# Kernel optimization log

Measured on AMD Instinct MI355X. Metric: run time of the kernel, lower is better.

Reference implementation:

```python
import jax, jax.numpy as jnp
import numpy as np

N_COG = 72  # 360 / delta_cog
N_RB = 72   # 360 / delta_rb
B, N, H = 64, 512, 128


def setup_inputs() -> dict:
    key = jax.random.key(0)
    k1, k2, k3, k4, k5, k6 = jax.random.split(key, 6)
    h_t = jax.random.normal(k1, (N, B, H), dtype=jnp.float32)
    r_mat = jax.random.randint(k2, (B, N, N), 0, N_RB, dtype=jnp.int32)
    d_mat = jax.random.uniform(k3, (B, N, N), dtype=jnp.float32)
    mask = jax.random.randint(k4, (B, N), 0, 2).astype(jnp.float32)
    cog_mat = jax.random.randint(k5, (B, N, N), 0, N_COG, dtype=jnp.int32)
    domain = jax.random.normal(k6, (N_COG, N_RB), dtype=jnp.float32)
    return {"h_t": h_t, "r_mat": r_mat, "d_mat": d_mat, "mask": mask,
            "cog_mat": cog_mat, "domain": domain}


def reference(h_t, r_mat, d_mat, mask, cog_mat, domain):
    # gather from learnable domain table, subtract distance, relu
    w = jax.nn.relu(domain[cog_mat, r_mat] - d_mat)          # [B, N, N]
    # pairwise mask (applied twice in the original, around normalization)
    m = mask[:, :, None] * mask[:, None, :]                   # [B, N, N]
    w = m * w
    # global-max normalize; torch uses .data.max() (no grad through max)
    w = w / jax.lax.stop_gradient(jnp.max(w))
    w = m * w
    # out[b,i,h] = sum_j w[b,i,j] * h_t[j,b,h]
    return jnp.einsum('bij,jbh->bih', w, h_t)                 # [B, N, H]
```

## Files before the change

kernel.cpp:

```cpp
#include <hip/hip_runtime.h>


#define B_   64
#define N_   512
#define H_   128
#define NCOG 72
#define NRB  72

typedef __bf16 bf16x8 __attribute__((ext_vector_type(8)));
typedef float  f32x4  __attribute__((ext_vector_type(4)));

__device__ __forceinline__ void async_copy16_nt(const void* g, void* l) {
    __builtin_amdgcn_global_load_lds(
        (const __attribute__((address_space(1))) void*)g,
        (__attribute__((address_space(3))) void*)l, 16, 0, 2);
}

__global__ __launch_bounds__(256) void k_transpose(const float* __restrict__ ht,
                                                   __bf16* __restrict__ T) {
    __shared__ __bf16 tile[32][136];
    const int jt = blockIdx.x * 32;
    const int b  = blockIdx.y;
    const int t  = threadIdx.x;
    {
        const int jj = t >> 3;
        const int h0 = (t & 7) << 4;
        const float* src = ht + ((size_t)(jt + jj) * B_ + b) * H_ + h0;
        float4 v0 = *(const float4*)(src + 0);
        float4 v1 = *(const float4*)(src + 4);
        float4 v2 = *(const float4*)(src + 8);
        float4 v3 = *(const float4*)(src + 12);
        __bf16* dst = &tile[jj][h0];
        dst[0]=(__bf16)v0.x; dst[1]=(__bf16)v0.y; dst[2]=(__bf16)v0.z; dst[3]=(__bf16)v0.w;
        dst[4]=(__bf16)v1.x; dst[5]=(__bf16)v1.y; dst[6]=(__bf16)v1.z; dst[7]=(__bf16)v1.w;
        dst[8]=(__bf16)v2.x; dst[9]=(__bf16)v2.y; dst[10]=(__bf16)v2.z; dst[11]=(__bf16)v2.w;
        dst[12]=(__bf16)v3.x; dst[13]=(__bf16)v3.y; dst[14]=(__bf16)v3.z; dst[15]=(__bf16)v3.w;
    }
    __syncthreads();
    {
        const int h  = t >> 1;
        const int j0 = (t & 1) << 4;
        union { bf16x8 v[2]; __bf16 e[16]; } ob;
        #pragma unroll
        for (int q = 0; q < 16; ++q) ob.e[q] = tile[j0 + q][h];
        __bf16* dst = T + ((size_t)b * H_ + h) * N_ + jt + j0;
        *(bf16x8*)(dst + 0) = ob.v[0];
        *(bf16x8*)(dst + 8) = ob.v[1];
    }
}

__global__ __launch_bounds__(512, 4) void k_main(const int* __restrict__ cog,
                                                 const int* __restrict__ rmat,
                                                 const float* __restrict__ dmat,
                                                 const float* __restrict__ mask,
                                                 const float* __restrict__ domain,
                                                 const __bf16* __restrict__ T,
                                                 float* __restrict__ out,
                                                 unsigned int* __restrict__ gmax) {
    __shared__ int   tiles[2 * 3 * 2048];
    __shared__ float sdom[NCOG * NRB];
    __shared__ float smask[N_];
    __shared__ float swmax[8];

    const int id    = blockIdx.x;
    const int xcd   = id & 7;
    const int i0idx = (id >> 3) & 7;
    const int bhi   = id >> 6;
    const int b     = xcd + 8 * bhi;
    const int i0    = i0idx * 64;

    const int t    = threadIdx.x;
    const int wave = t >> 6;
    const int lane = t & 63;

    for (int k = t; k < NCOG * NRB; k += 512) sdom[k] = domain[k];
    for (int k = t; k < N_; k += 512) smask[k] = mask[b * N_ + k];

    const size_t robase = ((size_t)b * N_ + i0) * N_;

    float wmax = 0.0f;

    if (wave >= 4) {
        const int pw   = wave - 4;
        const int csw4 = ((lane & 7) ^ (lane >> 3)) * 4;
        const size_t poff = (size_t)(lane >> 3) * N_ + csw4;

        #pragma unroll
        for (int q6 = 0; q6 < 6; ++q6) {
            const int q = pw * 6 + q6, a = q >> 3, c8 = q & 7;
            const size_t goff = robase + (size_t)(c8 * 8) * N_ + poff;
            const void* g = (a == 0) ? (const void*)(cog + goff)
                          : (a == 1) ? (const void*)(rmat + goff)
                                     : (const void*)(dmat + goff);
            async_copy16_nt(g, &tiles[a * 2048 + c8 * 256]);
        }
        __syncthreads();
        for (int s = 0; s < 16; ++s) {
            if (s + 1 < 16) {
                const int kk  = (s + 1) * 32;
                const int buf = (s + 1) & 1;
                #pragma unroll
                for (int q6 = 0; q6 < 6; ++q6) {
                    const int q = pw * 6 + q6, a = q >> 3, c8 = q & 7;
                    const size_t goff = robase + (size_t)(c8 * 8) * N_ + kk + poff;
                    const void* g = (a == 0) ? (const void*)(cog + goff)
                                  : (a == 1) ? (const void*)(rmat + goff)
                                             : (const void*)(dmat + goff);
                    async_copy16_nt(g, &tiles[buf * 6144 + a * 2048 + c8 * 256]);
                }
            }
            __syncthreads();
        }
    } else {
        const int quad = lane >> 4;
        const int lrow = lane & 15;
        const int row  = wave * 16 + lrow;
        const int g0   = (row * 8 + ((quad * 2)     ^ (row & 7))) * 4;
        const int g1   = (row * 8 + ((quad * 2 + 1) ^ (row & 7))) * 4;
        const __bf16* Tcol = T + (size_t)b * H_ * N_ + (size_t)lrow * N_ + quad * 8;

        f32x4 acc[8];
        #pragma unroll
        for (int i = 0; i < 8; ++i) acc[i] = (f32x4)0.0f;

        bf16x8 bfbuf[2][8];
        #pragma unroll
        for (int nt = 0; nt < 8; ++nt)
            bfbuf[0][nt] = *(const bf16x8*)(Tcol + (size_t)nt * 16 * N_);

        __syncthreads();
        #pragma unroll 2
        for (int s = 0; s < 16; ++s) {
            const int kk  = s * 32;
            const int cb  = s & 1;
            if (s + 1 < 16) {
                #pragma unroll
                for (int nt = 0; nt < 8; ++nt)
                    bfbuf[cb ^ 1][nt] = *(const bf16x8*)(Tcol + (size_t)nt * 16 * N_ + kk + 32);
            }
            const int jb = kk + quad * 8;
            const int* tb = tiles + cb * 6144;
            union { int4 v[2]; int   e[8]; } ci, ri;
            union { int4 v[2]; float e[8]; } di;
            ci.v[0] = *(const int4*)(tb + g0);        ci.v[1] = *(const int4*)(tb + g1);
            ri.v[0] = *(const int4*)(tb + 2048 + g0); ri.v[1] = *(const int4*)(tb + 2048 + g1);
            di.v[0] = *(const int4*)(tb + 4096 + g0); di.v[1] = *(const int4*)(tb + 4096 + g1);

            union { bf16x8 v8; __bf16 e[8]; } af;
            #pragma unroll
            for (int q = 0; q < 8; ++q) {
                float val = sdom[ci.e[q] * NRB + ri.e[q]] - di.e[q];
                val = fmaxf(val, 0.0f) * smask[jb + q];
                wmax = fmaxf(wmax, val);
                af.e[q] = (__bf16)val;
            }
            #pragma unroll
            for (int nt = 0; nt < 8; ++nt)
                acc[nt] = __builtin_amdgcn_mfma_f32_16x16x32_bf16(af.v8, bfbuf[cb][nt], acc[nt], 0, 0, 0);
            __syncthreads();
        }

        wmax *= smask[i0 + row];

        const int orow0 = i0 + wave * 16 + quad * 4;
        #pragma unroll
        for (int nt = 0; nt < 8; ++nt) {
            #pragma unroll
            for (int r = 0; r < 4; ++r)
                out[((size_t)b * N_ + orow0 + r) * H_ + nt * 16 + lrow] = acc[nt][r];
        }
    }

    #pragma unroll
    for (int off = 32; off > 0; off >>= 1)
        wmax = fmaxf(wmax, __shfl_down(wmax, off));
    if (lane == 0) swmax[wave] = wmax;
    __syncthreads();
    if (t == 0) {
        float m = swmax[0];
        #pragma unroll
        for (int w = 1; w < 8; ++w) m = fmaxf(m, swmax[w]);
        atomicMax(gmax, __float_as_uint(m));
    }
}

__global__ __launch_bounds__(256) void k_scale(float* __restrict__ out,
                                               const float* __restrict__ mask,
                                               const unsigned int* __restrict__ gmax) {
    const float inv = 1.0f / __uint_as_float(*gmax);
    const int idx = blockIdx.x * 256 + threadIdx.x;
    const float m = mask[idx >> 5] * inv;
    float4* p = (float4*)out;
    float4 v = p[idx];
    v.x *= m; v.y *= m; v.z *= m; v.w *= m;
    p[idx] = v;
}

extern "C" void kernel_launch(void* const* d_in, const int* in_sizes, int n_in,
                              void* d_out, int out_size, void* d_ws, size_t ws_size,
                              hipStream_t stream) {
    const float* ht     = (const float*)d_in[0];
    const int*   rmat   = (const int*)  d_in[1];
    const float* dmat   = (const float*)d_in[2];
    const float* mask   = (const float*)d_in[3];
    const int*   cog    = (const int*)  d_in[4];
    const float* domain = (const float*)d_in[5];
    float* out = (float*)d_out;

    unsigned int* gmax = (unsigned int*)d_ws;
    __bf16* T = (__bf16*)((char*)d_ws + 256);

    hipMemsetAsync(d_ws, 0, 256, stream);
    k_transpose<<<dim3(16, 64), 256, 0, stream>>>(ht, T);
    k_main<<<dim3(512), 512, 0, stream>>>(cog, rmat, dmat, mask, domain, T, out, gmax);
    k_scale<<<4096, 256, 0, stream>>>(out, mask, gmax);
}
```

Before: 234.7 us.

## Deepen producer-wave LDS prefetch pipeline to four buffers with fine-grained waitcnt

```diff
diff --git a/kernel.cpp b/kernel.cpp
--- a/kernel.cpp
+++ b/kernel.cpp
@@ -49,7 +49,7 @@
     }
 }
 
-__global__ __launch_bounds__(512, 4) void k_main(const int* __restrict__ cog,
+__global__ __launch_bounds__(512, 1) void k_main(const int* __restrict__ cog,
                                                  const int* __restrict__ rmat,
                                                  const float* __restrict__ dmat,
                                                  const float* __restrict__ mask,
@@ -57,7 +57,7 @@
                                                  const __bf16* __restrict__ T,
                                                  float* __restrict__ out,
                                                  unsigned int* __restrict__ gmax) {
-    __shared__ int   tiles[2 * 3 * 2048];
+    __shared__ int   tiles[4 * 3 * 2048];
     __shared__ float sdom[NCOG * NRB];
     __shared__ float smask[N_];
     __shared__ float swmax[8];
@@ -85,32 +85,38 @@
         const int csw4 = ((lane & 7) ^ (lane >> 3)) * 4;
         const size_t poff = (size_t)(lane >> 3) * N_ + csw4;
 
-        #pragma unroll
-        for (int q6 = 0; q6 < 6; ++q6) {
-            const int q = pw * 6 + q6, a = q >> 3, c8 = q & 7;
-            const size_t goff = robase + (size_t)(c8 * 8) * N_ + poff;
-            const void* g = (a == 0) ? (const void*)(cog + goff)
-                          : (a == 1) ? (const void*)(rmat + goff)
-                                     : (const void*)(dmat + goff);
-            async_copy16_nt(g, &tiles[a * 2048 + c8 * 256]);
+        #define ISSUE_BATCH(n)                                                      \
+            do {                                                                    \
+                const int kk_ = (n) * 32, buf_ = (n) & 3;                           \
+                _Pragma("unroll")                                                   \
+                for (int q6 = 0; q6 < 6; ++q6) {                                    \
+                    const int q = pw * 6 + q6, a = q >> 3, c8 = q & 7;              \
+                    const size_t goff = robase + (size_t)(c8 * 8) * N_ + kk_ + poff;\
+                    const void* g = (a == 0) ? (const void*)(cog + goff)            \
+                                  : (a == 1) ? (const void*)(rmat + goff)           \
+                                             : (const void*)(dmat + goff);         \
+                    async_copy16_nt(g, &tiles[buf_ * 6144 + a * 2048 + c8 * 256]);  \
+                }                                                                   \
+            } while (0)
+
+        ISSUE_BATCH(0);
+        ISSUE_BATCH(1);
+        ISSUE_BATCH(2);
+        asm volatile("s_waitcnt vmcnt(12) lgkmcnt(0)\n\ts_barrier" ::: "memory");
+
+        for (int s = 0; s < 16; ++s) {
+            if (s < 13) {
+                ISSUE_BATCH(s + 3);
+                asm volatile("s_waitcnt vmcnt(12)\n\ts_barrier" ::: "memory");
+            } else if (s == 13) {
+                asm volatile("s_waitcnt vmcnt(6)\n\ts_barrier" ::: "memory");
+            } else if (s == 14) {
+                asm volatile("s_waitcnt vmcnt(0)\n\ts_barrier" ::: "memory");
+            } else {
+                asm volatile("s_barrier" ::: "memory");
+            }
         }
-        __syncthreads();
-        for (int s = 0; s < 16; ++s) {
-            if (s + 1 < 16) {
-                const int kk  = (s + 1) * 32;
-                const int buf = (s + 1) & 1;
-                #pragma unroll
-                for (int q6 = 0; q6 < 6; ++q6) {
-                    const int q = pw * 6 + q6, a = q >> 3, c8 = q & 7;
-                    const size_t goff = robase + (size_t)(c8 * 8) * N_ + kk + poff;
-                    const void* g = (a == 0) ? (const void*)(cog + goff)
-                                  : (a == 1) ? (const void*)(rmat + goff)
-                                             : (const void*)(dmat + goff);
-                    async_copy16_nt(g, &tiles[buf * 6144 + a * 2048 + c8 * 256]);
-                }
-            }
-            __syncthreads();
-        }
+        #undef ISSUE_BATCH
     } else {
         const int quad = lane >> 4;
         const int lrow = lane & 15;
@@ -129,7 +135,7 @@
             bfbuf[0][nt] = *(const bf16x8*)(Tcol + (size_t)nt * 16 * N_);
 
         __syncthreads();
-        #pragma unroll 2
+        #pragma unroll 4
         for (int s = 0; s < 16; ++s) {
             const int kk  = s * 32;
             const int cb  = s & 1;
@@ -139,7 +145,7 @@
                     bfbuf[cb ^ 1][nt] = *(const bf16x8*)(Tcol + (size_t)nt * 16 * N_ + kk + 32);
             }
             const int jb = kk + quad * 8;
-            const int* tb = tiles + cb * 6144;
+            const int* tb = tiles + (s & 3) * 6144;
             union { int4 v[2]; int   e[8]; } ci, ri;
             union { int4 v[2]; float e[8]; } di;
             ci.v[0] = *(const int4*)(tb + g0);        ci.v[1] = *(const int4*)(tb + g1);
```

Result: no change. 232.3 us (-1.0%).
